# Kernel optimization log

Hardware: AMD Instinct MI355X
Metric: run time of the kernel (lower is better)

## Reference

```python
import jax, jax.numpy as jnp
import numpy as np

EMBED_DIM = 2048
NUM_HEADS = 16
HEAD_DIM = EMBED_DIM // NUM_HEADS
B, T = 4, 2048


def setup_inputs() -> dict:
    key = jax.random.key(0)
    ks = jax.random.split(key, 9)
    s = 1.0 / np.sqrt(EMBED_DIM)
    x = jax.random.normal(ks[0], (B, T, EMBED_DIM), dtype=jnp.float32)
    Wq = jax.random.normal(ks[1], (EMBED_DIM, EMBED_DIM), dtype=jnp.float32) * s
    bq = jnp.zeros((EMBED_DIM,), dtype=jnp.float32)
    Wk = jax.random.normal(ks[2], (EMBED_DIM, EMBED_DIM), dtype=jnp.float32) * s
    bk = jnp.zeros((EMBED_DIM,), dtype=jnp.float32)
    Wv = jax.random.normal(ks[3], (EMBED_DIM, EMBED_DIM), dtype=jnp.float32) * s
    bv = jnp.zeros((EMBED_DIM,), dtype=jnp.float32)
    Wo = jax.random.normal(ks[4], (EMBED_DIM, EMBED_DIM), dtype=jnp.float32) * s
    bo = jnp.zeros((EMBED_DIM,), dtype=jnp.float32)
    return {"x": x, "Wq": Wq, "bq": bq, "Wk": Wk, "bk": bk,
            "Wv": Wv, "bv": bv, "Wo": Wo, "bo": bo}


def reference(x, Wq, bq, Wk, bk, Wv, bv, Wo, bo):
    Bb, Tt, C = x.shape
    H, D = NUM_HEADS, C // NUM_HEADS
    # QKV projections (Linear: x @ W.T + b), reshape to [B, H, T, D]
    q = (jnp.einsum('btc,oc->bto', x, Wq) + bq).reshape(Bb, Tt, H, D).transpose(0, 2, 1, 3)
    k = (jnp.einsum('btc,oc->bto', x, Wk) + bk).reshape(Bb, Tt, H, D).transpose(0, 2, 1, 3)
    v = (jnp.einsum('btc,oc->bto', x, Wv) + bv).reshape(Bb, Tt, H, D).transpose(0, 2, 1, 3)
    logits = jnp.einsum('bhqd,bhkd->bhqk', q, k) / jnp.sqrt(jnp.float32(D))
    causal = jnp.triu(jnp.ones((Tt, Tt), dtype=bool), 1)  # True above diagonal
    logits = jnp.where(causal, -jnp.inf, logits)
    attn = jax.nn.softmax(logits, axis=-1)
    out = jnp.einsum('bhqk,bhkd->bhqd', attn, v)  # [B, H, T, D]
    out = out.transpose(0, 2, 1, 3).reshape(Bb, Tt, C)
    y = jnp.einsum('btc,oc->bto', out, Wo) + bo
    return y
```

## Files before the change

### kernel.cpp

```cpp
#include <hip/hip_runtime.h>
#include <hip/hip_bf16.h>
#include <cstdint>
#include <cstddef>

typedef __attribute__((ext_vector_type(8))) short short8;
typedef __attribute__((ext_vector_type(4))) short short4_;
typedef __attribute__((ext_vector_type(4))) float floatx4;
typedef __attribute__((ext_vector_type(4))) unsigned short ushort4_;

#define MFMA16(a, b, c) __builtin_amdgcn_mfma_f32_16x16x32_bf16((a), (b), (c), 0, 0, 0)

__device__ __forceinline__ unsigned short f2bf(float f) {
  __hip_bfloat16 h = __float2bfloat16(f);
  return *reinterpret_cast<unsigned short*>(&h);
}

__device__ __forceinline__ void gl_lds16(const void* g, void* lds) {
  __builtin_amdgcn_global_load_lds(
      (const __attribute__((address_space(1))) void*)g,
      (__attribute__((address_space(3))) void*)lds, 16, 0, 0);
}

__global__ void cast_f32_bf16(const float* __restrict__ in, __hip_bfloat16* __restrict__ out) {
  const int i = (blockIdx.x * 256 + threadIdx.x) * 4;
  const float4 v = *reinterpret_cast<const float4*>(in + i);
  ushort4_ o = { f2bf(v.x), f2bf(v.y), f2bf(v.z), f2bf(v.w) };
  *reinterpret_cast<ushort4_*>(out + i) = o;
}

template <int MODE>
__global__ __launch_bounds__(256, 2)
void gemm_bt(const __hip_bfloat16* __restrict__ A, const __hip_bfloat16* __restrict__ Bw,
             const float* __restrict__ bias, void* __restrict__ Cout,
             int M, int N, int K) {
  __shared__ __align__(16) __hip_bfloat16 As[128 * 32];
  __shared__ __align__(16) __hip_bfloat16 Bs[128 * 32];
  const int tid = threadIdx.x;
  const int w = tid >> 6, lane = tid & 63;
  const int g = lane >> 4, c16 = lane & 15;
  const int nbn = N >> 7;
  const int bm = blockIdx.x / nbn, bn = blockIdx.x % nbn;
  const int wr = w >> 1, wc = w & 1;

  floatx4 acc[4][4] = {};

  const int srow = lane >> 2;
  const int sseg = (lane & 3) * 8;
  const int nkt = K >> 5;
  for (int kt = 0; kt < nkt; ++kt) {
    const int kb = kt * 32;
#pragma unroll
    for (int i = 0; i < 2; ++i) {
      const int cidx = w + i * 4;
      const int row = cidx * 16 + srow;
      gl_lds16(A + (size_t)(bm * 128 + row) * K + kb + sseg, As + cidx * 512);
      gl_lds16(Bw + (size_t)(bn * 128 + row) * K + kb + sseg, Bs + cidx * 512);
    }
    __syncthreads();
    short8 af[4], bf[4];
#pragma unroll
    for (int m = 0; m < 4; ++m)
      af[m] = *reinterpret_cast<const short8*>(As + (wr * 64 + m * 16 + c16) * 32 + g * 8);
#pragma unroll
    for (int n = 0; n < 4; ++n)
      bf[n] = *reinterpret_cast<const short8*>(Bs + (wc * 64 + n * 16 + c16) * 32 + g * 8);
#pragma unroll
    for (int m = 0; m < 4; ++m)
#pragma unroll
      for (int n = 0; n < 4; ++n)
        acc[m][n] = MFMA16(af[m], bf[n], acc[m][n]);
    __syncthreads();
  }

#pragma unroll
  for (int n = 0; n < 4; ++n) {
    const int colg = bn * 128 + wc * 64 + n * 16 + c16;
    const float bv = bias[colg];
#pragma unroll
    for (int m = 0; m < 4; ++m) {
      const int rowg = bm * 128 + wr * 64 + m * 16 + g * 4;
      if (MODE == 0) {
        __hip_bfloat16* C = (__hip_bfloat16*)Cout;
#pragma unroll
        for (int j = 0; j < 4; ++j)
          C[(size_t)(rowg + j) * N + colg] = __float2bfloat16(acc[m][n][j] + bv);
      } else if (MODE == 1) {
        __hip_bfloat16* C = (__hip_bfloat16*)Cout;
        const int bb = rowg >> 11, t0 = rowg & 2047;
        ushort4_ pk = { f2bf(acc[m][n][0] + bv), f2bf(acc[m][n][1] + bv),
                        f2bf(acc[m][n][2] + bv), f2bf(acc[m][n][3] + bv) };
        *reinterpret_cast<ushort4_*>(C + ((size_t)bb * 2048 + colg) * 2048 + t0) = pk;
      } else {
        float* C = (float*)Cout;
#pragma unroll
        for (int j = 0; j < 4; ++j)
          C[(size_t)(rowg + j) * N + colg] = acc[m][n][j] + bv;
      }
    }
  }
}

__global__ __launch_bounds__(256, 2)
void attn_fwd4(const __hip_bfloat16* __restrict__ Q, const __hip_bfloat16* __restrict__ K,
               const __hip_bfloat16* __restrict__ Vt, __hip_bfloat16* __restrict__ ctx) {
  constexpr int T = 2048, C = 2048, D = 128;
  __shared__ __align__(16) __hip_bfloat16 Ks[64][136];
  __shared__ __align__(16) __hip_bfloat16 Vs[128][64];
  __shared__ __align__(16) __hip_bfloat16 Pl[4][32][64];

  const int tid = threadIdx.x;
  const int w = tid >> 6, lane = tid & 63;
  const int g = lane >> 4, c16 = lane & 15;

  const int bid = blockIdx.x;
  const int swz = (bid & 7) * 128 + (bid >> 3);
  const int bh = swz >> 4, qb = 15 - (swz & 15);
  const int b = bh >> 4, h = bh & 15;
  const int wq = qb * 128 + w * 32;

  const __hip_bfloat16* Qh = Q + (size_t)b * T * C + h * D;
  const __hip_bfloat16* Kh = K + (size_t)b * T * C + h * D;
  const __hip_bfloat16* Vh = Vt + (size_t)bh * D * T;

  short8 qf[2][4];
#pragma unroll
  for (int m = 0; m < 2; ++m)
#pragma unroll
    for (int kk = 0; kk < 4; ++kk)
      qf[m][kk] = *reinterpret_cast<const short8*>(Qh + (size_t)(wq + m * 16 + c16) * C + kk * 32 + g * 8);

  floatx4 acc[2][8] = {};
  float mrow[2] = {-INFINITY, -INFINITY};
  float lrow[2] = {0.f, 0.f};

  const float scale = 0.08838834764831845f;
  const int krow = tid >> 4, kcol = (tid & 15) * 8;
  const int vrow = tid >> 3;
  const int vslot = (tid & 7) ^ (vrow & 7);
  const int vgcol = (tid & 7) * 8;

  short8 kr[4], vr[4];
  auto gloadK = [&](int kb) {
#pragma unroll
    for (int p = 0; p < 4; ++p)
      kr[p] = *reinterpret_cast<const short8*>(Kh + (size_t)(kb + p * 16 + krow) * C + kcol);
  };
  auto gloadV = [&](int kb) {
#pragma unroll
    for (int p = 0; p < 4; ++p)
      vr[p] = *reinterpret_cast<const short8*>(Vh + (size_t)(p * 32 + vrow) * T + kb + vgcol);
  };

  __hip_bfloat16 (*Pq)[64] = Pl[w];
  const int nkt = qb * 2 + 2;
  gloadK(0);
  gloadV(0);

  for (int kt = 0; kt < nkt; ++kt) {
    const int kb = kt * 64;
    __syncthreads();
#pragma unroll
    for (int p = 0; p < 4; ++p)
      *reinterpret_cast<short8*>(&Ks[p * 16 + krow][kcol]) = kr[p];
#pragma unroll
    for (int p = 0; p < 4; ++p)
      *reinterpret_cast<short8*>(&Vs[p * 32 + vrow][vslot * 8]) = vr[p];
    __syncthreads();

    const bool hasnext = (kt + 1 < nkt);
    const bool part = (kb <= wq + 31);
    if (hasnext) gloadK(kb + 64);

    if (part) {
      const bool needmask = (kb + 63 > wq);
      floatx4 s[2][4] = {};
      __builtin_amdgcn_s_setprio(1);
#pragma unroll
      for (int n = 0; n < 4; ++n)
#pragma unroll
        for (int kk = 0; kk < 4; ++kk) {
          short8 kf = *reinterpret_cast<const short8*>(&Ks[n * 16 + c16][kk * 32 + g * 8]);
          s[0][n] = MFMA16(kf, qf[0][kk], s[0][n]);
          s[1][n] = MFMA16(kf, qf[1][kk], s[1][n]);
        }
      __builtin_amdgcn_s_setprio(0);
      float vmax[2];
#pragma unroll
      for (int m = 0; m < 2; ++m) {
        const int q = wq + m * 16 + c16;
        float vm = -INFINITY;
#pragma unroll
        for (int n = 0; n < 4; ++n)
#pragma unroll
          for (int j = 0; j < 4; ++j) {
            float a = s[m][n][j] * scale;
            if (needmask && (kb + n * 16 + g * 4 + j > q)) a = -INFINITY;
            s[m][n][j] = a;
            vm = fmaxf(vm, a);
          }
        vm = fmaxf(vm, __shfl_xor(vm, 16));
        vm = fmaxf(vm, __shfl_xor(vm, 32));
        vmax[m] = vm;
      }
      const float grow = fmaxf(vmax[0] - mrow[0], vmax[1] - mrow[1]);
      const bool nore = __all(grow <= 8.0f);
#pragma unroll
      for (int m = 0; m < 2; ++m) {
        const float mn = nore ? mrow[m] : fmaxf(mrow[m], vmax[m]);
        float rs = 0.f;
#pragma unroll
        for (int n = 0; n < 4; ++n) {
          float p0 = __expf(s[m][n][0] - mn), p1 = __expf(s[m][n][1] - mn);
          float p2 = __expf(s[m][n][2] - mn), p3 = __expf(s[m][n][3] - mn);
          rs += (p0 + p1) + (p2 + p3);
          ushort4_ pk = { f2bf(p0), f2bf(p1), f2bf(p2), f2bf(p3) };
          *reinterpret_cast<ushort4_*>(&Pq[m * 16 + c16][((4 * n + g) ^ c16) * 4]) = pk;
        }
        rs += __shfl_xor(rs, 16);
        rs += __shfl_xor(rs, 32);
        if (nore) {
          lrow[m] += rs;
        } else {
          const float sc = __expf(mrow[m] - mn);
          lrow[m] = lrow[m] * sc + rs;
          mrow[m] = mn;
#pragma unroll
          for (int dt = 0; dt < 8; ++dt)
#pragma unroll
            for (int j = 0; j < 4; ++j) acc[m][dt][j] *= sc;
        }
      }
    }
    if (hasnext) gloadV(kb + 64);
    if (part) {
      short8 pb[2][2];
#pragma unroll
      for (int m = 0; m < 2; ++m)
#pragma unroll
        for (int ks = 0; ks < 2; ++ks) {
          short4_ lo = *reinterpret_cast<const short4_*>(&Pq[m * 16 + c16][((8 * ks + 2 * g) ^ c16) * 4]);
          short4_ hi = *reinterpret_cast<const short4_*>(&Pq[m * 16 + c16][((8 * ks + 2 * g + 1) ^ c16) * 4]);
          short8 r;
          r[0] = lo[0]; r[1] = lo[1]; r[2] = lo[2]; r[3] = lo[3];
          r[4] = hi[0]; r[5] = hi[1]; r[6] = hi[2]; r[7] = hi[3];
          pb[m][ks] = r;
        }
      __builtin_amdgcn_s_setprio(1);
#pragma unroll
      for (int dt = 0; dt < 8; ++dt)
#pragma unroll
        for (int ks = 0; ks < 2; ++ks) {
          const int pslot = ((ks * 4 + g) ^ (c16 & 7)) * 8;
          short8 vf = *reinterpret_cast<const short8*>(&Vs[dt * 16 + c16][pslot]);
          acc[0][dt] = MFMA16(vf, pb[0][ks], acc[0][dt]);
          acc[1][dt] = MFMA16(vf, pb[1][ks], acc[1][dt]);
        }
      __builtin_amdgcn_s_setprio(0);
    }
  }

#pragma unroll
  for (int m = 0; m < 2; ++m) {
    const float inv = 1.0f / lrow[m];
    const size_t row = (size_t)b * T + wq + m * 16 + c16;
#pragma unroll
    for (int dt = 0; dt < 8; ++dt) {
      ushort4_ o = { f2bf(acc[m][dt][0] * inv), f2bf(acc[m][dt][1] * inv),
                     f2bf(acc[m][dt][2] * inv), f2bf(acc[m][dt][3] * inv) };
      *reinterpret_cast<ushort4_*>(ctx + row * C + h * D + dt * 16 + g * 4) = o;
    }
  }
}

extern "C" void kernel_launch(void* const* d_in, const int* in_sizes, int n_in,
                              void* d_out, int out_size, void* d_ws, size_t ws_size,
                              hipStream_t stream) {
  const float* x  = (const float*)d_in[0];
  const float* Wq = (const float*)d_in[1];
  const float* bq = (const float*)d_in[2];
  const float* Wk = (const float*)d_in[3];
  const float* bk = (const float*)d_in[4];
  const float* Wv = (const float*)d_in[5];
  const float* bv = (const float*)d_in[6];
  const float* Wo = (const float*)d_in[7];
  const float* bo = (const float*)d_in[8];

  const int M = 8192, N = 2048, K = 2048;
  const size_t MB = 1u << 20;
  char* ws = (char*)d_ws;
  __hip_bfloat16* xb  = (__hip_bfloat16*)(ws);
  __hip_bfloat16* wqb = (__hip_bfloat16*)(ws + 32 * MB);
  __hip_bfloat16* wkb = (__hip_bfloat16*)(ws + 40 * MB);
  __hip_bfloat16* wvb = (__hip_bfloat16*)(ws + 48 * MB);
  __hip_bfloat16* wob = (__hip_bfloat16*)(ws + 56 * MB);
  __hip_bfloat16* Qb  = (__hip_bfloat16*)(ws + 64 * MB);
  __hip_bfloat16* Kb  = (__hip_bfloat16*)(ws + 96 * MB);
  __hip_bfloat16* Vtb = (__hip_bfloat16*)(ws + 128 * MB);
  if (ws_size < 160 * MB) return;

  cast_f32_bf16<<<(M * N) / 1024, 256, 0, stream>>>(x, xb);
  cast_f32_bf16<<<(N * K) / 1024, 256, 0, stream>>>(Wq, wqb);
  cast_f32_bf16<<<(N * K) / 1024, 256, 0, stream>>>(Wk, wkb);
  cast_f32_bf16<<<(N * K) / 1024, 256, 0, stream>>>(Wv, wvb);
  cast_f32_bf16<<<(N * K) / 1024, 256, 0, stream>>>(Wo, wob);

  const dim3 gg((M / 128) * (N / 128));
  gemm_bt<0><<<gg, 256, 0, stream>>>(xb, wqb, bq, Qb, M, N, K);
  gemm_bt<0><<<gg, 256, 0, stream>>>(xb, wkb, bk, Kb, M, N, K);
  gemm_bt<1><<<gg, 256, 0, stream>>>(xb, wvb, bv, Vtb, M, N, K);

  attn_fwd4<<<64 * 16, 256, 0, stream>>>(Qb, Kb, Vtb, xb);

  gemm_bt<2><<<gg, 256, 0, stream>>>(xb, wob, bo, d_out, M, N, K);
}
```

Measured before the change: 544.1 us.

## Rewrite projection GEMMs as 256x256 tiles with 4-stage LDS pipeline

Replaces the 128x128 single-buffered GEMM with a 256x256-tile, 512-thread kernel. It uses a 4-slot LDS ring fed by async global-to-LDS loads with vmcnt-based waits, XOR-swizzled LDS layout to avoid bank conflicts, block-index swizzling for L2 locality, and s_setprio around the MFMA bursts. The goal is to overlap memory loads with MFMA work and raise arithmetic intensity in the four projection GEMMs. The kernel now needs 128KB of LDS and more accumulator registers. It also relies on fixed shape assumptions (N/256 = 8 tile columns in the swizzle).

```diff
diff --git a/kernel.cpp b/kernel.cpp
--- a/kernel.cpp
+++ b/kernel.cpp
@@ -29,56 +29,85 @@
 }
 
 template <int MODE>
-__global__ __launch_bounds__(256, 2)
-void gemm_bt(const __hip_bfloat16* __restrict__ A, const __hip_bfloat16* __restrict__ Bw,
+__global__ __launch_bounds__(512, 2)
+void gemm256(const __hip_bfloat16* __restrict__ Ap, const __hip_bfloat16* __restrict__ Bp,
              const float* __restrict__ bias, void* __restrict__ Cout,
              int M, int N, int K) {
-  __shared__ __align__(16) __hip_bfloat16 As[128 * 32];
-  __shared__ __align__(16) __hip_bfloat16 Bs[128 * 32];
+  __shared__ __align__(16) __hip_bfloat16 SA[4][256 * 32];
+  __shared__ __align__(16) __hip_bfloat16 SB[4][256 * 32];
+
   const int tid = threadIdx.x;
-  const int w = tid >> 6, lane = tid & 63;
+  const int wid = tid >> 6, lane = tid & 63;
+  const int wr = wid >> 2, wc = wid & 3;
   const int g = lane >> 4, c16 = lane & 15;
-  const int nbn = N >> 7;
-  const int bm = blockIdx.x / nbn, bn = blockIdx.x % nbn;
-  const int wr = w >> 1, wc = w & 1;
-
-  floatx4 acc[4][4] = {};
+
+  const int swzb = (blockIdx.x & 7) * 32 + (blockIdx.x >> 3);
+  const int bm = swzb >> 3, bn = swzb & 7;
 
   const int srow = lane >> 2;
-  const int sseg = (lane & 3) * 8;
-  const int nkt = K >> 5;
-  for (int kt = 0; kt < nkt; ++kt) {
+  const int slog = (lane & 3) ^ ((lane >> 3) & 3);
+  const int swz = c16 * 32 + (g ^ ((c16 >> 1) & 3)) * 8;
+
+  floatx4 acc[8][4] = {};
+
+  auto stage = [&](int kt) {
     const int kb = kt * 32;
+    const int slot = kt & 3;
 #pragma unroll
     for (int i = 0; i < 2; ++i) {
-      const int cidx = w + i * 4;
-      const int row = cidx * 16 + srow;
-      gl_lds16(A + (size_t)(bm * 128 + row) * K + kb + sseg, As + cidx * 512);
-      gl_lds16(Bw + (size_t)(bn * 128 + row) * K + kb + sseg, Bs + cidx * 512);
-    }
-    __syncthreads();
-    short8 af[4], bf[4];
-#pragma unroll
-    for (int m = 0; m < 4; ++m)
-      af[m] = *reinterpret_cast<const short8*>(As + (wr * 64 + m * 16 + c16) * 32 + g * 8);
+      const int rbase = i * 128 + wid * 16;
+      gl_lds16(Ap + (size_t)(bm * 256 + rbase + srow) * K + kb + slog * 8,
+               SA[slot] + rbase * 32);
+      gl_lds16(Bp + (size_t)(bn * 256 + rbase + srow) * K + kb + slog * 8,
+               SB[slot] + rbase * 32);
+    }
+  };
+
+  auto compute = [&](int slot) {
+    const __hip_bfloat16* sa = SA[slot];
+    const __hip_bfloat16* sb = SB[slot];
+    short8 af[8], bf[4];
+#pragma unroll
+    for (int m = 0; m < 8; ++m)
+      af[m] = *reinterpret_cast<const short8*>(sa + wr * 4096 + m * 512 + swz);
 #pragma unroll
     for (int n = 0; n < 4; ++n)
-      bf[n] = *reinterpret_cast<const short8*>(Bs + (wc * 64 + n * 16 + c16) * 32 + g * 8);
-#pragma unroll
-    for (int m = 0; m < 4; ++m)
+      bf[n] = *reinterpret_cast<const short8*>(sb + wc * 2048 + n * 512 + swz);
+    __builtin_amdgcn_s_setprio(1);
+#pragma unroll
+    for (int m = 0; m < 8; ++m)
 #pragma unroll
       for (int n = 0; n < 4; ++n)
         acc[m][n] = MFMA16(af[m], bf[n], acc[m][n]);
-    __syncthreads();
+    __builtin_amdgcn_s_setprio(0);
+  };
+
+  const int nkt = K >> 5;
+  stage(0); stage(1); stage(2);
+
+  for (int kt = 0; kt < nkt - 3; ++kt) {
+    asm volatile("s_waitcnt vmcnt(8)" ::: "memory");
+    __builtin_amdgcn_s_barrier();
+    stage(kt + 3);
+    compute(kt & 3);
   }
+  asm volatile("s_waitcnt vmcnt(8)" ::: "memory");
+  __builtin_amdgcn_s_barrier();
+  compute((nkt - 3) & 3);
+  asm volatile("s_waitcnt vmcnt(4)" ::: "memory");
+  __builtin_amdgcn_s_barrier();
+  compute((nkt - 2) & 3);
+  asm volatile("s_waitcnt vmcnt(0)" ::: "memory");
+  __builtin_amdgcn_s_barrier();
+  compute((nkt - 1) & 3);
 
 #pragma unroll
   for (int n = 0; n < 4; ++n) {
-    const int colg = bn * 128 + wc * 64 + n * 16 + c16;
+    const int colg = bn * 256 + wc * 64 + n * 16 + c16;
     const float bv = bias[colg];
 #pragma unroll
-    for (int m = 0; m < 4; ++m) {
-      const int rowg = bm * 128 + wr * 64 + m * 16 + g * 4;
+    for (int m = 0; m < 8; ++m) {
+      const int rowg = bm * 256 + wr * 128 + m * 16 + g * 4;
       if (MODE == 0) {
         __hip_bfloat16* C = (__hip_bfloat16*)Cout;
 #pragma unroll
@@ -304,12 +333,12 @@
   cast_f32_bf16<<<(N * K) / 1024, 256, 0, stream>>>(Wv, wvb);
   cast_f32_bf16<<<(N * K) / 1024, 256, 0, stream>>>(Wo, wob);
 
-  const dim3 gg((M / 128) * (N / 128));
-  gemm_bt<0><<<gg, 256, 0, stream>>>(xb, wqb, bq, Qb, M, N, K);
-  gemm_bt<0><<<gg, 256, 0, stream>>>(xb, wkb, bk, Kb, M, N, K);
-  gemm_bt<1><<<gg, 256, 0, stream>>>(xb, wvb, bv, Vtb, M, N, K);
+  const dim3 gg((M / 256) * (N / 256));
+  gemm256<0><<<gg, 512, 0, stream>>>(xb, wqb, bq, Qb, M, N, K);
+  gemm256<0><<<gg, 512, 0, stream>>>(xb, wkb, bk, Kb, M, N, K);
+  gemm256<1><<<gg, 512, 0, stream>>>(xb, wvb, bv, Vtb, M, N, K);
 
   attn_fwd4<<<64 * 16, 256, 0, stream>>>(Qb, Kb, Vtb, xb);
 
-  gemm_bt<2><<<gg, 256, 0, stream>>>(xb, wob, bo, d_out, M, N, K);
-}
+  gemm256<2><<<gg, 512, 0, stream>>>(xb, wob, bo, d_out, M, N, K);
+}
```

New measurement: 534.2 us. About the same (-1.8%).
